# Performance work log

Hardware: AMD Instinct MI355X
Metric: run time of the kernel (lower is better)

## Reference

```python
import jax, jax.numpy as jnp
import numpy as np

NUM_HEADS = 16
NEG = -1e9


def setup_inputs() -> dict:
    key = jax.random.key(0)
    ks = jax.random.split(key, 9)
    B, S, D = 1, 4096, 1024
    s = 1.0 / np.sqrt(D)
    return {
        "x": jax.random.normal(ks[0], (B, S, D), dtype=jnp.float32),
        "wq": jax.random.normal(ks[1], (D, D), dtype=jnp.float32) * s,
        "bq": jax.random.normal(ks[2], (D,), dtype=jnp.float32) * s,
        "wk": jax.random.normal(ks[3], (D, D), dtype=jnp.float32) * s,
        "bk": jax.random.normal(ks[4], (D,), dtype=jnp.float32) * s,
        "wv": jax.random.normal(ks[5], (D, D), dtype=jnp.float32) * s,
        "bv": jax.random.normal(ks[6], (D,), dtype=jnp.float32) * s,
        "wo": jax.random.normal(ks[7], (D, D), dtype=jnp.float32) * s,
        "bo": jax.random.normal(ks[8], (D,), dtype=jnp.float32) * s,
    }


def reference(x, wq, bq, wk, bk, wv, bv, wo, bo):
    B, S, D = x.shape
    H = NUM_HEADS
    hs = D // H
    # torch Linear: y = x @ W^T + b
    q = x @ wq.T + bq
    k = x @ wk.T + bk
    v = x @ wv.T + bv
    # [B, S, D] -> [B, H, S, hs]
    q = q.reshape(B, S, H, hs).transpose(0, 2, 1, 3)
    k = k.reshape(B, S, H, hs).transpose(0, 2, 1, 3)
    v = v.reshape(B, S, H, hs).transpose(0, 2, 1, 3)
    scores = jnp.einsum("bhqd,bhkd->bhqk", q, k) / jnp.sqrt(jnp.asarray(hs, x.dtype))
    causal = jnp.tril(jnp.ones((S, S), dtype=bool))  # True = keep
    scores = jnp.where(causal, scores, jnp.asarray(NEG, x.dtype))
    weights = jax.nn.softmax(scores, axis=-1)
    out = jnp.einsum("bhqk,bhkd->bhqd", weights, v)
    out = out.transpose(0, 2, 1, 3).reshape(B, S, D)
    return out @ wo.T + bo
```

## Files before the change

kernel.cpp:

```cpp
#include <hip/hip_runtime.h>

#define SEQ 4096
#define DM  1024
#define NH  16
#define HS  64
#define LDQK 2048

typedef __attribute__((ext_vector_type(8))) _Float16 f16x8;
typedef __attribute__((ext_vector_type(4))) _Float16 f16x4;
typedef __attribute__((ext_vector_type(4))) float    f32x4;

#define MFMA16(a, b, c) __builtin_amdgcn_mfma_f32_16x16x32_f16((a), (b), (c), 0, 0, 0)

#define DPP_ROR_F(x, N) __int_as_float(__builtin_amdgcn_update_dpp( \
    0, __float_as_int(x), 0x120 + (N), 0xF, 0xF, false))

__device__ __forceinline__ float red16_add(float x) {
    x += DPP_ROR_F(x, 1);
    x += DPP_ROR_F(x, 2);
    x += DPP_ROR_F(x, 4);
    x += DPP_ROR_F(x, 8);
    return x;
}

__global__ __launch_bounds__(256) void cast_all(
    const float* __restrict__ x,
    const float* __restrict__ wq, const float* __restrict__ wk,
    const float* __restrict__ wv, const float* __restrict__ wo,
    _Float16* __restrict__ xb, _Float16* __restrict__ wqkb,
    _Float16* __restrict__ wvb, _Float16* __restrict__ wob)
{
    const float* s; _Float16* d; int i;
    if (blockIdx.y == 0) {
        s = x; d = xb;
        i = blockIdx.x * 1024 + threadIdx.x * 4;
    } else {
        int wsel = blockIdx.x >> 10;
        int bx   = blockIdx.x & 1023;
        switch (wsel) {
            case 0:  s = wq; d = wqkb;               break;
            case 1:  s = wk; d = wqkb + (1u << 20);  break;
            case 2:  s = wv; d = wvb;                break;
            default: s = wo; d = wob;                break;
        }
        i = bx * 1024 + threadIdx.x * 4;
    }
    float4 v = *reinterpret_cast<const float4*>(s + i);
    f16x4 o = {(_Float16)v.x, (_Float16)v.y, (_Float16)v.z, (_Float16)v.w};
    *reinterpret_cast<f16x4*>(d + i) = o;
}

#define GPAD 72

template <int BIAS_ROW, typename OUT_T>
__global__ __launch_bounds__(256, 2) void gemm_bt_f16(
    const _Float16* __restrict__ A,
    const _Float16* __restrict__ W,
    const float*    __restrict__ bias_lo,
    const float*    __restrict__ bias_hi,
    OUT_T* __restrict__ C,
    int M, int N, int K,
    float scale_lo, float scale_hi, int nsplit)
{
    __shared__ _Float16 As[64][GPAD];
    __shared__ _Float16 Bs[128][GPAD];

    const int t    = threadIdx.x;
    const int w    = t >> 6;
    const int lane = t & 63;
    const int q    = lane >> 4;
    const int l    = lane & 15;
    const int m0   = blockIdx.y * 64;
    const int n0   = blockIdx.x * 128;
    const int wm   = (w & 1) * 32;
    const int wn   = (w >> 1) * 64;

    const float* bias  = (n0 < nsplit) ? bias_lo : bias_hi;
    const int    nbase = (n0 < nsplit) ? 0 : nsplit;
    const float  scale = (n0 < nsplit) ? scale_lo : scale_hi;

    const int ar = t >> 2, ac = (t & 3) * 16;
    const int br = t >> 1, bc = (t & 1) * 32;
    const _Float16* gA = A + (size_t)(m0 + ar) * K + ac;
    const _Float16* gW = W + (size_t)(n0 + br) * K + bc;

    uint4 ra0 = *reinterpret_cast<const uint4*>(gA);
    uint4 ra1 = *reinterpret_cast<const uint4*>(gA + 8);
    uint4 rb0 = *reinterpret_cast<const uint4*>(gW);
    uint4 rb1 = *reinterpret_cast<const uint4*>(gW + 8);
    uint4 rb2 = *reinterpret_cast<const uint4*>(gW + 16);
    uint4 rb3 = *reinterpret_cast<const uint4*>(gW + 24);

    f32x4 acc[2][4];
    #pragma unroll
    for (int i = 0; i < 2; ++i)
        #pragma unroll
        for (int j = 0; j < 4; ++j) acc[i][j] = (f32x4){0.f, 0.f, 0.f, 0.f};

    for (int k0 = 0; k0 < K; k0 += 64) {
        __syncthreads();
        *reinterpret_cast<uint4*>(&As[ar][ac])      = ra0;
        *reinterpret_cast<uint4*>(&As[ar][ac + 8])  = ra1;
        *reinterpret_cast<uint4*>(&Bs[br][bc])      = rb0;
        *reinterpret_cast<uint4*>(&Bs[br][bc + 8])  = rb1;
        *reinterpret_cast<uint4*>(&Bs[br][bc + 16]) = rb2;
        *reinterpret_cast<uint4*>(&Bs[br][bc + 24]) = rb3;
        if (k0 + 64 < K) {
            ra0 = *reinterpret_cast<const uint4*>(gA + k0 + 64);
            ra1 = *reinterpret_cast<const uint4*>(gA + k0 + 72);
            rb0 = *reinterpret_cast<const uint4*>(gW + k0 + 64);
            rb1 = *reinterpret_cast<const uint4*>(gW + k0 + 72);
            rb2 = *reinterpret_cast<const uint4*>(gW + k0 + 80);
            rb3 = *reinterpret_cast<const uint4*>(gW + k0 + 88);
        }
        __syncthreads();

        #pragma unroll
        for (int ks = 0; ks < 64; ks += 32) {
            f16x8 af[2], bf[4];
            #pragma unroll
            for (int i = 0; i < 2; ++i)
                af[i] = *reinterpret_cast<const f16x8*>(&As[wm + i * 16 + l][ks + q * 8]);
            #pragma unroll
            for (int j = 0; j < 4; ++j)
                bf[j] = *reinterpret_cast<const f16x8*>(&Bs[wn + j * 16 + l][ks + q * 8]);
            #pragma unroll
            for (int i = 0; i < 2; ++i)
                #pragma unroll
                for (int j = 0; j < 4; ++j)
                    acc[i][j] = MFMA16(af[i], bf[j], acc[i][j]);
        }
    }

    #pragma unroll
    for (int i = 0; i < 2; ++i) {
        #pragma unroll
        for (int j = 0; j < 4; ++j) {
            int gnb = n0 + wn + j * 16 + l;
            float bc2 = BIAS_ROW ? 0.f : bias[gnb - nbase];
            #pragma unroll
            for (int r = 0; r < 4; ++r) {
                int gm = m0 + wm + i * 16 + q * 4 + r;
                float bb = BIAS_ROW ? bias[gm] : bc2;
                C[(size_t)gm * N + gnb] = (OUT_T)((acc[i][j][r] + bb) * scale);
            }
        }
    }
}

#define APAD 72

__global__ __launch_bounds__(256, 2) void attn_mfma(
    const _Float16* __restrict__ Qg,
    const _Float16* __restrict__ Kg,
    const _Float16* __restrict__ Vt,
    _Float16* __restrict__ O)
{
    __shared__ _Float16 Qs[64][APAD];
    __shared__ _Float16 Ks[64][APAD];
    __shared__ _Float16 Vs[64][APAD];
    __shared__ _Float16 Ps[64][APAD];

    const int t    = threadIdx.x;
    const int h    = blockIdx.x;
    const int bx   = blockIdx.y;
    const int w    = t >> 6;
    const int lane = t & 63;
    const int q    = lane >> 4;
    const int l    = lane & 15;
    const int sr   = t >> 3;
    const int sc   = (t & 7) * 8;

    for (int phase = 0; phase < 2; ++phase) {
        const int qb = phase ? (63 - bx) : bx;

        __syncthreads();
        *reinterpret_cast<uint4*>(&Qs[sr][sc]) =
            *reinterpret_cast<const uint4*>(Qg + (size_t)(qb * 64 + sr) * LDQK + h * 64 + sc);
        *reinterpret_cast<uint4*>(&Qs[sr + 32][sc]) =
            *reinterpret_cast<const uint4*>(Qg + (size_t)(qb * 64 + sr + 32) * LDQK + h * 64 + sc);

        uint4 kr0 = *reinterpret_cast<const uint4*>(Kg + (size_t)(sr) * LDQK + h * 64 + sc);
        uint4 kr1 = *reinterpret_cast<const uint4*>(Kg + (size_t)(sr + 32) * LDQK + h * 64 + sc);
        uint4 vr0 = *reinterpret_cast<const uint4*>(Vt + (size_t)(h * 64 + sr) * SEQ + sc);
        uint4 vr1 = *reinterpret_cast<const uint4*>(Vt + (size_t)(h * 64 + sr + 32) * SEQ + sc);

        float l_acc[4] = {0.f, 0.f, 0.f, 0.f};
        f32x4 oacc[4];
        #pragma unroll
        for (int nt = 0; nt < 4; ++nt) oacc[nt] = (f32x4){0.f, 0.f, 0.f, 0.f};

        __syncthreads();
        f16x8 aq0 = *reinterpret_cast<const f16x8*>(&Qs[w * 16 + l][q * 8]);
        f16x8 aq1 = *reinterpret_cast<const f16x8*>(&Qs[w * 16 + l][32 + q * 8]);

        const int qrow_base = qb * 64 + w * 16 + q * 4;

        for (int kt = 0; kt <= qb; ++kt) {
            __syncthreads();
            *reinterpret_cast<uint4*>(&Ks[sr][sc])      = kr0;
            *reinterpret_cast<uint4*>(&Ks[sr + 32][sc]) = kr1;
            *reinterpret_cast<uint4*>(&Vs[sr][sc])      = vr0;
            *reinterpret_cast<uint4*>(&Vs[sr + 32][sc]) = vr1;
            if (kt < qb) {
                kr0 = *reinterpret_cast<const uint4*>(
                    Kg + (size_t)((kt + 1) * 64 + sr) * LDQK + h * 64 + sc);
                kr1 = *reinterpret_cast<const uint4*>(
                    Kg + (size_t)((kt + 1) * 64 + sr + 32) * LDQK + h * 64 + sc);
                vr0 = *reinterpret_cast<const uint4*>(
                    Vt + (size_t)(h * 64 + sr) * SEQ + (kt + 1) * 64 + sc);
                vr1 = *reinterpret_cast<const uint4*>(
                    Vt + (size_t)(h * 64 + sr + 32) * SEQ + (kt + 1) * 64 + sc);
            }
            __syncthreads();

            f32x4 s[4];
            __builtin_amdgcn_s_setprio(1);
            #pragma unroll
            for (int jt = 0; jt < 4; ++jt) {
                f16x8 bk0 = *reinterpret_cast<const f16x8*>(&Ks[4 * l + jt][q * 8]);
                f16x8 bk1 = *reinterpret_cast<const f16x8*>(&Ks[4 * l + jt][32 + q * 8]);
                f32x4 z = (f32x4){0.f, 0.f, 0.f, 0.f};
                z = MFMA16(aq0, bk0, z);
                z = MFMA16(aq1, bk1, z);
                s[jt] = z;
            }
            __builtin_amdgcn_s_setprio(0);

            const bool diag = (kt == qb);

            #pragma unroll
            for (int r = 0; r < 4; ++r) {
                float p0 = s[0][r], p1 = s[1][r], p2 = s[2][r], p3 = s[3][r];
                if (diag) {
                    const int qg = qrow_base + r;
                    const int kg = kt * 64 + 4 * l;
                    p0 = (kg + 0 <= qg) ? p0 : -1e30f;
                    p1 = (kg + 1 <= qg) ? p1 : -1e30f;
                    p2 = (kg + 2 <= qg) ? p2 : -1e30f;
                    p3 = (kg + 3 <= qg) ? p3 : -1e30f;
                }
                p0 = __builtin_amdgcn_exp2f(p0 - 4.f);
                p1 = __builtin_amdgcn_exp2f(p1 - 4.f);
                p2 = __builtin_amdgcn_exp2f(p2 - 4.f);
                p3 = __builtin_amdgcn_exp2f(p3 - 4.f);
                l_acc[r] += (p0 + p1) + (p2 + p3);
                f16x4 pk = {(_Float16)p0, (_Float16)p1, (_Float16)p2, (_Float16)p3};
                *reinterpret_cast<f16x4*>(&Ps[w * 16 + q * 4 + r][4 * l]) = pk;
            }

            f16x8 ap0 = *reinterpret_cast<const f16x8*>(&Ps[w * 16 + l][q * 8]);
            f16x8 ap1 = *reinterpret_cast<const f16x8*>(&Ps[w * 16 + l][32 + q * 8]);
            __builtin_amdgcn_s_setprio(1);
            #pragma unroll
            for (int nt = 0; nt < 4; ++nt) {
                f16x8 bv0 = *reinterpret_cast<const f16x8*>(&Vs[nt * 16 + l][q * 8]);
                f16x8 bv1 = *reinterpret_cast<const f16x8*>(&Vs[nt * 16 + l][32 + q * 8]);
                oacc[nt] = MFMA16(ap0, bv0, oacc[nt]);
                oacc[nt] = MFMA16(ap1, bv1, oacc[nt]);
            }
            __builtin_amdgcn_s_setprio(0);
        }

        #pragma unroll
        for (int r = 0; r < 4; ++r) {
            float inv = 1.f / red16_add(l_acc[r]);
            size_t row = (size_t)(qb * 64 + w * 16 + q * 4 + r) * DM + h * 64;
            #pragma unroll
            for (int nt = 0; nt < 4; ++nt)
                O[row + nt * 16 + l] = (_Float16)(oacc[nt][r] * inv);
        }
    }
}

extern "C" void kernel_launch(void* const* d_in, const int* in_sizes, int n_in,
                              void* d_out, int out_size, void* d_ws, size_t ws_size,
                              hipStream_t stream)
{
    const float* x  = (const float*)d_in[0];
    const float* wq = (const float*)d_in[1];
    const float* bq = (const float*)d_in[2];
    const float* wk = (const float*)d_in[3];
    const float* bk = (const float*)d_in[4];
    const float* wv = (const float*)d_in[5];
    const float* bv = (const float*)d_in[6];
    const float* wo = (const float*)d_in[7];
    const float* bo = (const float*)d_in[8];
    float* out = (float*)d_out;

    char* ws = (char*)d_ws;
    _Float16* xb   = (_Float16*)(ws);
    _Float16* wqkb = (_Float16*)(ws + (8ull  << 20));
    _Float16* wvb  = (_Float16*)(ws + (12ull << 20));
    _Float16* wob  = (_Float16*)(ws + (14ull << 20));
    _Float16* QKb  = (_Float16*)(ws + (16ull << 20));
    _Float16* Vtb  = (_Float16*)(ws + (32ull << 20));
    _Float16* Ab   = (_Float16*)(ws + (40ull << 20));

    cast_all<<<dim3(SEQ * DM / 1024, 2), dim3(256), 0, stream>>>(
        x, wq, wk, wv, wo, xb, wqkb, wvb, wob);

    gemm_bt_f16<0, _Float16><<<dim3(2048 / 128, SEQ / 64), dim3(256), 0, stream>>>(
        xb, wqkb, bq, bk, QKb, SEQ, 2048, DM,
        0.18033688011112042f, 1.0f, 1024);

    gemm_bt_f16<1, _Float16><<<dim3(SEQ / 128, DM / 64), dim3(256), 0, stream>>>(
        wvb, xb, bv, bv, Vtb, DM, SEQ, DM, 1.0f, 1.0f, 1 << 30);

    attn_mfma<<<dim3(NH, 32), dim3(256), 0, stream>>>(QKb, QKb + 1024, Vtb, Ab);

    gemm_bt_f16<0, float><<<dim3(DM / 128, SEQ / 64), dim3(256), 0, stream>>>(
        Ab, wob, bo, bo, out, SEQ, DM, DM, 1.0f, 1.0f, 1 << 30);
}
```

Before: 214.3 us.

## Double-buffer K/V tiles in LDS and use one barrier per iteration

K and V tiles in the attention kernel now live in two LDS buffers. The next tile is written into the spare buffer while the current one is consumed, so each iteration needs one __syncthreads instead of two. The K tile is also stored as [jt][l] so the B-operand reads are contiguous rows, which may change the bank-conflict pattern. In exchange, LDS use per block roughly doubles for K and V, which could limit occupancy, and the prefetch logic now runs two tiles ahead.

Measured after the change: 213.9 us. No clear change (-0.2%).

```diff
diff --git a/kernel.cpp b/kernel.cpp
--- a/kernel.cpp
+++ b/kernel.cpp
@@ -157,8 +157,8 @@
     _Float16* __restrict__ O)
 {
     __shared__ _Float16 Qs[64][APAD];
-    __shared__ _Float16 Ks[64][APAD];
-    __shared__ _Float16 Vs[64][APAD];
+    __shared__ _Float16 Ks[2][4][16][APAD];
+    __shared__ _Float16 Vs[2][64][APAD];
     __shared__ _Float16 Ps[64][APAD];
 
     const int t    = threadIdx.x;
@@ -170,6 +170,8 @@
     const int l    = lane & 15;
     const int sr   = t >> 3;
     const int sc   = (t & 7) * 8;
+    const int kj   = sr & 3;
+    const int kn   = sr >> 2;
 
     for (int phase = 0; phase < 2; ++phase) {
         const int qb = phase ? (63 - bx) : bx;
@@ -184,6 +186,16 @@
         uint4 kr1 = *reinterpret_cast<const uint4*>(Kg + (size_t)(sr + 32) * LDQK + h * 64 + sc);
         uint4 vr0 = *reinterpret_cast<const uint4*>(Vt + (size_t)(h * 64 + sr) * SEQ + sc);
         uint4 vr1 = *reinterpret_cast<const uint4*>(Vt + (size_t)(h * 64 + sr + 32) * SEQ + sc);
+        *reinterpret_cast<uint4*>(&Ks[0][kj][kn][sc])     = kr0;
+        *reinterpret_cast<uint4*>(&Ks[0][kj][kn + 8][sc]) = kr1;
+        *reinterpret_cast<uint4*>(&Vs[0][sr][sc])         = vr0;
+        *reinterpret_cast<uint4*>(&Vs[0][sr + 32][sc])    = vr1;
+        if (qb > 0) {
+            kr0 = *reinterpret_cast<const uint4*>(Kg + (size_t)(64 + sr) * LDQK + h * 64 + sc);
+            kr1 = *reinterpret_cast<const uint4*>(Kg + (size_t)(64 + sr + 32) * LDQK + h * 64 + sc);
+            vr0 = *reinterpret_cast<const uint4*>(Vt + (size_t)(h * 64 + sr) * SEQ + 64 + sc);
+            vr1 = *reinterpret_cast<const uint4*>(Vt + (size_t)(h * 64 + sr + 32) * SEQ + 64 + sc);
+        }
 
         float l_acc[4] = {0.f, 0.f, 0.f, 0.f};
         f32x4 oacc[4];
@@ -197,29 +209,30 @@
         const int qrow_base = qb * 64 + w * 16 + q * 4;
 
         for (int kt = 0; kt <= qb; ++kt) {
-            __syncthreads();
-            *reinterpret_cast<uint4*>(&Ks[sr][sc])      = kr0;
-            *reinterpret_cast<uint4*>(&Ks[sr + 32][sc]) = kr1;
-            *reinterpret_cast<uint4*>(&Vs[sr][sc])      = vr0;
-            *reinterpret_cast<uint4*>(&Vs[sr + 32][sc]) = vr1;
+            const int p = kt & 1;
             if (kt < qb) {
-                kr0 = *reinterpret_cast<const uint4*>(
-                    Kg + (size_t)((kt + 1) * 64 + sr) * LDQK + h * 64 + sc);
-                kr1 = *reinterpret_cast<const uint4*>(
-                    Kg + (size_t)((kt + 1) * 64 + sr + 32) * LDQK + h * 64 + sc);
-                vr0 = *reinterpret_cast<const uint4*>(
-                    Vt + (size_t)(h * 64 + sr) * SEQ + (kt + 1) * 64 + sc);
-                vr1 = *reinterpret_cast<const uint4*>(
-                    Vt + (size_t)(h * 64 + sr + 32) * SEQ + (kt + 1) * 64 + sc);
-            }
-            __syncthreads();
+                *reinterpret_cast<uint4*>(&Ks[p ^ 1][kj][kn][sc])     = kr0;
+                *reinterpret_cast<uint4*>(&Ks[p ^ 1][kj][kn + 8][sc]) = kr1;
+                *reinterpret_cast<uint4*>(&Vs[p ^ 1][sr][sc])         = vr0;
+                *reinterpret_cast<uint4*>(&Vs[p ^ 1][sr + 32][sc])    = vr1;
+                if (kt + 1 < qb) {
+                    kr0 = *reinterpret_cast<const uint4*>(
+                        Kg + (size_t)((kt + 2) * 64 + sr) * LDQK + h * 64 + sc);
+                    kr1 = *reinterpret_cast<const uint4*>(
+                        Kg + (size_t)((kt + 2) * 64 + sr + 32) * LDQK + h * 64 + sc);
+                    vr0 = *reinterpret_cast<const uint4*>(
+                        Vt + (size_t)(h * 64 + sr) * SEQ + (kt + 2) * 64 + sc);
+                    vr1 = *reinterpret_cast<const uint4*>(
+                        Vt + (size_t)(h * 64 + sr + 32) * SEQ + (kt + 2) * 64 + sc);
+                }
+            }
 
             f32x4 s[4];
             __builtin_amdgcn_s_setprio(1);
             #pragma unroll
             for (int jt = 0; jt < 4; ++jt) {
-                f16x8 bk0 = *reinterpret_cast<const f16x8*>(&Ks[4 * l + jt][q * 8]);
-                f16x8 bk1 = *reinterpret_cast<const f16x8*>(&Ks[4 * l + jt][32 + q * 8]);
+                f16x8 bk0 = *reinterpret_cast<const f16x8*>(&Ks[p][jt][l][q * 8]);
+                f16x8 bk1 = *reinterpret_cast<const f16x8*>(&Ks[p][jt][l][32 + q * 8]);
                 f32x4 z = (f32x4){0.f, 0.f, 0.f, 0.f};
                 z = MFMA16(aq0, bk0, z);
                 z = MFMA16(aq1, bk1, z);
@@ -254,12 +267,14 @@
             __builtin_amdgcn_s_setprio(1);
             #pragma unroll
             for (int nt = 0; nt < 4; ++nt) {
-                f16x8 bv0 = *reinterpret_cast<const f16x8*>(&Vs[nt * 16 + l][q * 8]);
-                f16x8 bv1 = *reinterpret_cast<const f16x8*>(&Vs[nt * 16 + l][32 + q * 8]);
+                f16x8 bv0 = *reinterpret_cast<const f16x8*>(&Vs[p][nt * 16 + l][q * 8]);
+                f16x8 bv1 = *reinterpret_cast<const f16x8*>(&Vs[p][nt * 16 + l][32 + q * 8]);
                 oacc[nt] = MFMA16(ap0, bv0, oacc[nt]);
                 oacc[nt] = MFMA16(ap1, bv1, oacc[nt]);
             }
             __builtin_amdgcn_s_setprio(0);
+
+            __syncthreads();
         }
 
         #pragma unroll
```
